# Kernel optimization log

Measured on AMD Instinct MI355X. Metric: run time of the kernel, lower is better.

Reference implementation:

```python
import jax, jax.numpy as jnp
import numpy as np

NDIM = 3
N = 192
DX = 1.0 / N          # uniform unit box
T_REF = 300.0         # reference temperature [K]
MU_REF = 1.8e-5       # reference viscosity [Pa s]
PR = 0.72             # Prandtl number
CP = 1005.0           # specific heat [J/kg/K]


def _ddx(f, axis):
    # 2nd-order central difference, periodic BC
    return (jnp.roll(f, -1, axis) - jnp.roll(f, 1, axis)) / (2.0 * DX)


def _gradient(f):
    # scalar [N,N,N] -> [NDIM, N,N,N]
    return jnp.stack([_ddx(f, a) for a in range(NDIM)], axis=0)


def _divergence(v):
    # vector [NDIM, N,N,N] -> [N,N,N]
    out = _ddx(v[0], 0)
    for a in range(1, NDIM):
        out = out + _ddx(v[a], a)
    return out


def _viscosity(T_dim):
    return MU_REF * (T_dim / T_REF) ** 0.7


def _conductivity(T_dim):
    return _viscosity(T_dim) * CP / PR


def setup_inputs() -> dict:
    key = jax.random.key(0)
    k1, k2 = jax.random.split(key)
    u = jax.random.normal(k1, (NDIM, N, N, N), dtype=jnp.float32)
    # nondimensional temperature, kept positive for the power-law viscosity
    T = jax.random.uniform(k2, (N, N, N), dtype=jnp.float32, minval=0.5, maxval=1.5)
    return {"u": u, "T": T}


def reference(u, T):
    # --- stress tensor ---
    mu = _viscosity(T * T_REF)                                   # [N,N,N]
    # gradu[i, j] = d u_i / d x_j
    gradu = jnp.stack([_gradient(u[i]) for i in range(NDIM)], 0)  # [3,3,N,N,N]
    divu = jnp.einsum('ii...->...', gradu)                        # trace -> [N,N,N]
    S = 0.5 * (gradu + jnp.swapaxes(gradu, 0, 1))                 # symmetrized
    eye = jnp.eye(NDIM, dtype=u.dtype)[:, :, None, None, None]
    tau = 2.0 * mu * S - (2.0 / 3.0) * mu * divu * eye            # [3,3,N,N,N]

    # --- heat flux ---
    k = _conductivity(T * T_REF)
    heat_flux = -k * _gradient(T)                                 # [3,N,N,N]

    # --- assemble RHS: [mass(=0), momentum(3), energy] ---
    momentum = jnp.stack([_divergence(tau[i]) for i in range(NDIM)], 0)
    energy = -_divergence(heat_flux)
    for i in range(NDIM):
        energy = energy + _divergence(tau[i] * u[i])
    zero = jnp.zeros_like(T)
    return jnp.concatenate([zero[None], momentum, energy[None]], axis=0)
```

## Files before the change

kernel.cpp:

```cpp
#include <hip/hip_runtime.h>

#define N  192
#define N2 (N * N)
#define N3 (N * N * N)

#define TX 32
#define TY 8
#define NT 256
#define ZC 12
#define GX (N / TX)
#define GY (N / TY)
#define GZ (N / ZC)
#define NBLK (GX * GY * GZ)
#define UX (TX + 4)
#define UY (TY + 4)
#define UP (UX * UY)
#define FX (TX + 2)
#define FY (TY + 2)
#define FP (FX * FY)

static constexpr float INV2DX     = (float)N / 2.0f;
static constexpr float SCALE2     = INV2DX * INV2DX;
static constexpr float MU_REF_F   = 1.8e-5f;
static constexpr float CP_OVER_PR = 1005.0f / 0.72f;
static constexpr float TWO_THIRDS = 2.0f / 3.0f;

__device__ __forceinline__ int wrapN(int a) {
    if (a < 0)  a += N;
    if (a >= N) a -= N;
    return a;
}

struct Flux { float t00, t01, t02, t11, t12, t22, F0, F1, F2; };

__device__ __forceinline__ Flux flux_eval_reg(const float4 zm, const float4 cc,
                                              const float4 zp,
                                              const float4* __restrict__ uC, int c)
{
    const float4 xp = uC[c + 1],  xm = uC[c - 1];
    const float4 yp = uC[c + UX], ym = uC[c - UX];

    const float d00 = zp.x - zm.x;
    const float d01 = yp.x - ym.x;
    const float d02 = xp.x - xm.x;
    const float d10 = zp.y - zm.y;
    const float d11 = yp.y - ym.y;
    const float d12 = xp.y - xm.y;
    const float d20 = zp.z - zm.z;
    const float d21 = yp.z - ym.z;
    const float d22 = xp.z - xm.z;
    const float dT0 = zp.w - zm.w;
    const float dT1 = yp.w - ym.w;
    const float dT2 = xp.w - xm.w;

    const float mu   = MU_REF_F * __powf(cc.w, 0.7f);
    const float mu2  = mu + mu;
    const float divu = d00 + d11 + d22;
    const float lam  = -TWO_THIRDS * mu * divu;

    Flux f;
    f.t00 = mu2 * d00 + lam;
    f.t11 = mu2 * d11 + lam;
    f.t22 = mu2 * d22 + lam;
    f.t01 = mu * (d01 + d10);
    f.t02 = mu * (d02 + d20);
    f.t12 = mu * (d12 + d21);
    const float kc = mu * CP_OVER_PR;
    f.F0 = kc * dT0 + f.t00 * cc.x + f.t01 * cc.y + f.t02 * cc.z;
    f.F1 = kc * dT1 + f.t01 * cc.x + f.t11 * cc.y + f.t12 * cc.z;
    f.F2 = kc * dT2 + f.t02 * cc.x + f.t12 * cc.y + f.t22 * cc.z;
    return f;
}

__device__ __forceinline__ Flux flux_eval_lds(const float4* __restrict__ uM,
                                              const float4* __restrict__ uC,
                                              const float4* __restrict__ uP, int c)
{
    return flux_eval_reg(uM[c], uC[c], uP[c], uC, c);
}

__device__ __forceinline__ void sf_store(float4* __restrict__ sY, float4* __restrict__ sX,
                                         int fi, const Flux& f)
{
    sY[fi] = make_float4(f.t01, f.t11, f.t12, f.F1);
    sX[fi] = make_float4(f.t02, f.t12, f.t22, f.F2);
}

__global__ __launch_bounds__(NT)
void diffusion_zmarch_kernel(const float* __restrict__ u,
                             const float* __restrict__ Tp,
                             float* __restrict__ out)
{
    __shared__ float4 su4[3][UP];
    __shared__ float4 sfY[FP];
    __shared__ float4 sfX[FP];

    const int id  = (int)blockIdx.x;
    const int nid = (id & 7) * (NBLK / 8) + (id >> 3);
    const int bzB = nid / (GX * GY);
    const int rem = nid % (GX * GY);
    const int bx  = (rem % GX) * TX;
    const int by  = (rem / GX) * TY;
    const int z0  = bzB * ZC;

    const int tx  = threadIdx.x & (TX - 1);
    const int ty  = threadIdx.x >> 5;
    const int tid = (int)threadIdx.x;

    const float* __restrict__ u0 = u;
    const float* __restrict__ u1 = u + N3;
    const float* __restrict__ u2 = u + 2 * N3;

    const int cu = (ty + 2) * UX + (tx + 2);
    const int fi = (ty + 1) * FX + (tx + 1);

    int hfx = -1, hfy = -1;
    if (tid < TX)                 { hfy = 0;      hfx = 1 + tid; }
    else if (tid < 2 * TX)        { hfy = FY - 1; hfx = 1 + tid - TX; }
    else if (tid < 2 * TX + TY)   { hfx = 0;      hfy = 1 + tid - 2 * TX; }
    else if (tid < 2 * (TX + TY)) { hfx = FX - 1; hfy = 1 + tid - 2 * TX - TY; }
    const bool hasH = (hfx >= 0);
    const int hcu = (hfy + 1) * UX + (hfx + 1);
    const int hfi = hfy * FX + hfx;

    const int  q0   = tid;
    const int  q1   = tid + NT;
    const bool has2 = (q1 < UP);
    int ro0, ro1 = 0;
    {
        const int ux = q0 % UX, uy = q0 / UX;
        ro0 = wrapN(by + uy - 2) * N + wrapN(bx + ux - 2);
    }
    if (has2) {
        const int ux = q1 % UX, uy = q1 / UX;
        ro1 = wrapN(by + uy - 2) * N + wrapN(bx + ux - 2);
    }

#define STAGE_DIRECT(slot, zw)                                              \
    do {                                                                    \
        const int base_ = (zw) * N2;                                        \
        {  const int g_ = base_ + ro0;                                      \
           su4[slot][q0] = make_float4(u0[g_], u1[g_], u2[g_], Tp[g_]); }   \
        if (has2) {                                                         \
           const int g_ = base_ + ro1;                                      \
           su4[slot][q1] = make_float4(u0[g_], u1[g_], u2[g_], Tp[g_]); }   \
    } while (0)

    STAGE_DIRECT(0, wrapN(z0 - 2));
    STAGE_DIRECT(1, wrapN(z0 - 1));
    STAGE_DIRECT(2, z0);
    __syncthreads();

    float t00m, t01m, t02m, F0m;
    {
        const Flux fM = flux_eval_lds(su4[0], su4[1], su4[2], cu);
        t00m = fM.t00; t01m = fM.t01; t02m = fM.t02; F0m = fM.F0;
    }
    __syncthreads();
    STAGE_DIRECT(0, z0 + 1);
    __syncthreads();

    float t00c, t01c, t02c, F0c;
    {
        const Flux fC = flux_eval_lds(su4[1], su4[2], su4[0], cu);
        t00c = fC.t00; t01c = fC.t01; t02c = fC.t02; F0c = fC.F0;
        sf_store(sfY, sfX, fi, fC);
        if (hasH) {
            const Flux h = flux_eval_lds(su4[1], su4[2], su4[0], hcu);
            sf_store(sfY, sfX, hfi, h);
        }
    }
    __syncthreads();
    STAGE_DIRECT(1, z0 + 2);
    __syncthreads();

    float4 rzm = su4[2][cu];
    float4 rcc = su4[0][cu];
    float4 hzm, hcc;
    if (hasH) { hzm = su4[2][hcu]; hcc = su4[0][hcu]; }

    float4 *pC = su4[0], *pP = su4[1], *pW = su4[2];

    int idx = z0 * N2 + (by + ty) * N + bx + tx;
    int zw  = z0 + 3; if (zw >= N) zw -= N;

    for (int it = 0; it < ZC; ++it) {
        const bool pref = (it <= ZC - 2);
        float4 r0, r1;
        if (pref) {
            const int base_ = zw * N2;
            { const int g_ = base_ + ro0;
              r0 = make_float4(u0[g_], u1[g_], u2[g_], Tp[g_]); }
            if (has2) {
              const int g_ = base_ + ro1;
              r1 = make_float4(u0[g_], u1[g_], u2[g_], Tp[g_]); }
        }

        const float4 yp = sfY[fi + FX], ym = sfY[fi - FX];
        const float4 xp = sfX[fi + 1],  xm = sfX[fi - 1];
        const float4 own = pP[cu];
        float4 hown;
        if (hasH) hown = pP[hcu];

        asm volatile("s_waitcnt lgkmcnt(0)\n\ts_barrier" ::: "memory");

        const Flux fp_ = flux_eval_reg(rzm, rcc, own, pC, cu);
        Flux h;
        if (hasH) h = flux_eval_reg(hzm, hcc, hown, pC, hcu);

        const float m0 = (fp_.t00 - t00m) + (yp.x - ym.x) + (xp.x - xm.x);
        const float m1 = (fp_.t01 - t01m) + (yp.y - ym.y) + (xp.y - xm.y);
        const float m2 = (fp_.t02 - t02m) + (yp.z - ym.z) + (xp.z - xm.z);
        const float en = (fp_.F0  - F0m)  + (yp.w - ym.w) + (xp.w - xm.w);

        sf_store(sfY, sfX, fi, fp_);
        if (hasH) sf_store(sfY, sfX, hfi, h);
        if (pref) { pW[q0] = r0; if (has2) pW[q1] = r1; }

        __builtin_nontemporal_store(m0 * SCALE2, &out[1 * N3 + idx]);
        __builtin_nontemporal_store(m1 * SCALE2, &out[2 * N3 + idx]);
        __builtin_nontemporal_store(m2 * SCALE2, &out[3 * N3 + idx]);
        __builtin_nontemporal_store(en * SCALE2, &out[4 * N3 + idx]);

        asm volatile("s_waitcnt lgkmcnt(0)\n\ts_barrier" ::: "memory");

        t00m = t00c; t01m = t01c; t02m = t02c; F0m = F0c;
        t00c = fp_.t00; t01c = fp_.t01; t02c = fp_.t02; F0c = fp_.F0;
        rzm = rcc; rcc = own;
        if (hasH) { hzm = hcc; hcc = hown; }
        float4* t = pC; pC = pP; pP = pW; pW = t;
        idx += N2;
        if (++zw >= N) zw = 0;
    }
#undef STAGE_DIRECT
}

extern "C" void kernel_launch(void* const* d_in, const int* in_sizes, int n_in,
                              void* d_out, int out_size, void* d_ws, size_t ws_size,
                              hipStream_t stream)
{
    const float* u   = (const float*)d_in[0];
    const float* T   = (const float*)d_in[1];
    float*       out = (float*)d_out;

    hipMemsetAsync(out, 0, (size_t)N3 * sizeof(float), stream);

    hipLaunchKernelGGL(diffusion_zmarch_kernel, dim3(NBLK), dim3(NT), 0, stream,
                       u, T, out);
}
```

Before: 101.4 us.

## Process two z-planes per march iteration with double-buffered flux tiles

Restructures the z-march so each loop iteration computes fluxes for two planes and writes two output planes, using a second pair of shared flux buffers. All LDS reads for both planes are hoisted before a single barrier, and two input planes are prefetched per iteration, halving the number of barrier pairs per block. It also adds a launch-bounds occupancy hint of 3 blocks. The cost is much higher register pressure from the extra live float4 neighbours and a larger shared-memory footprint, which may limit occupancy or cause spills.

```diff
diff --git a/kernel.cpp b/kernel.cpp
--- a/kernel.cpp
+++ b/kernel.cpp
@@ -8,6 +8,7 @@
 #define TY 8
 #define NT 256
 #define ZC 12
+#define NIT (ZC / 2)
 #define GX (N / TX)
 #define GY (N / TY)
 #define GZ (N / ZC)
@@ -33,13 +34,11 @@
 
 struct Flux { float t00, t01, t02, t11, t12, t22, F0, F1, F2; };
 
-__device__ __forceinline__ Flux flux_eval_reg(const float4 zm, const float4 cc,
-                                              const float4 zp,
-                                              const float4* __restrict__ uC, int c)
-{
-    const float4 xp = uC[c + 1],  xm = uC[c - 1];
-    const float4 yp = uC[c + UX], ym = uC[c - UX];
-
+__device__ __forceinline__ Flux flux_eval(const float4 zm, const float4 cc,
+                                          const float4 zp,
+                                          const float4 xp, const float4 xm,
+                                          const float4 yp, const float4 ym)
+{
     const float d00 = zp.x - zm.x;
     const float d01 = yp.x - ym.x;
     const float d02 = xp.x - xm.x;
@@ -72,28 +71,22 @@
     return f;
 }
 
-__device__ __forceinline__ Flux flux_eval_lds(const float4* __restrict__ uM,
-                                              const float4* __restrict__ uC,
-                                              const float4* __restrict__ uP, int c)
-{
-    return flux_eval_reg(uM[c], uC[c], uP[c], uC, c);
-}
-
-__device__ __forceinline__ void sf_store(float4* __restrict__ sY, float4* __restrict__ sX,
-                                         int fi, const Flux& f)
-{
-    sY[fi] = make_float4(f.t01, f.t11, f.t12, f.F1);
-    sX[fi] = make_float4(f.t02, f.t12, f.t22, f.F2);
-}
-
-__global__ __launch_bounds__(NT)
-void diffusion_zmarch_kernel(const float* __restrict__ u,
-                             const float* __restrict__ Tp,
-                             float* __restrict__ out)
+__device__ __forceinline__ Flux flux_eval_at(const float4* __restrict__ uM,
+                                             const float4* __restrict__ uC,
+                                             const float4* __restrict__ uP, int c)
+{
+    return flux_eval(uM[c], uC[c], uP[c], uC[c + 1], uC[c - 1],
+                     uC[c + UX], uC[c - UX]);
+}
+
+__global__ __launch_bounds__(NT, 3)
+void diffusion_zmarch2_kernel(const float* __restrict__ u,
+                              const float* __restrict__ Tp,
+                              float* __restrict__ out)
 {
     __shared__ float4 su4[3][UP];
-    __shared__ float4 sfY[FP];
-    __shared__ float4 sfX[FP];
+    __shared__ float4 sfAY[FP], sfAX[FP];
+    __shared__ float4 sfBY[FP], sfBX[FP];
 
     const int id  = (int)blockIdx.x;
     const int nid = (id & 7) * (NBLK / 8) + (id >> 3);
@@ -153,7 +146,7 @@
 
     float t00m, t01m, t02m, F0m;
     {
-        const Flux fM = flux_eval_lds(su4[0], su4[1], su4[2], cu);
+        const Flux fM = flux_eval_at(su4[0], su4[1], su4[2], cu);
         t00m = fM.t00; t01m = fM.t01; t02m = fM.t02; F0m = fM.F0;
     }
     __syncthreads();
@@ -161,76 +154,120 @@
     __syncthreads();
 
     float t00c, t01c, t02c, F0c;
+    float4 rA, rB;
+    float4 hA = make_float4(0,0,0,0), hB = make_float4(0,0,0,0);
     {
-        const Flux fC = flux_eval_lds(su4[1], su4[2], su4[0], cu);
+        const Flux fC = flux_eval_at(su4[1], su4[2], su4[0], cu);
         t00c = fC.t00; t01c = fC.t01; t02c = fC.t02; F0c = fC.F0;
-        sf_store(sfY, sfX, fi, fC);
-        if (hasH) {
-            const Flux h = flux_eval_lds(su4[1], su4[2], su4[0], hcu);
-            sf_store(sfY, sfX, hfi, h);
-        }
+        sfAY[fi] = make_float4(fC.t01, fC.t11, fC.t12, fC.F1);
+        sfAX[fi] = make_float4(fC.t02, fC.t12, fC.t22, fC.F2);
+        if (hasH) {
+            const Flux h = flux_eval_at(su4[1], su4[2], su4[0], hcu);
+            sfAY[hfi] = make_float4(h.t01, h.t11, h.t12, h.F1);
+            sfAX[hfi] = make_float4(h.t02, h.t12, h.t22, h.F2);
+            hA = su4[2][hcu];
+            hB = su4[0][hcu];
+        }
+        rA = su4[2][cu];
+        rB = su4[0][cu];
     }
     __syncthreads();
     STAGE_DIRECT(1, z0 + 2);
-    __syncthreads();
-
-    float4 rzm = su4[2][cu];
-    float4 rcc = su4[0][cu];
-    float4 hzm, hcc;
-    if (hasH) { hzm = su4[2][hcu]; hcc = su4[0][hcu]; }
-
-    float4 *pC = su4[0], *pP = su4[1], *pW = su4[2];
+    STAGE_DIRECT(2, z0 + 3);
+    __syncthreads();
+
+    float4 *pA = su4[0], *pB = su4[1], *pC = su4[2];
 
     int idx = z0 * N2 + (by + ty) * N + bx + tx;
-    int zw  = z0 + 3; if (zw >= N) zw -= N;
-
-    for (int it = 0; it < ZC; ++it) {
-        const bool pref = (it <= ZC - 2);
-        float4 r0, r1;
+
+    for (int k = 0; k < NIT; ++k) {
+        const int  z    = z0 + 2 * k;
+        const bool pref = (k < NIT - 1);
+
+        float4 r4a, r4b, r5a, r5b;
         if (pref) {
-            const int base_ = zw * N2;
-            { const int g_ = base_ + ro0;
-              r0 = make_float4(u0[g_], u1[g_], u2[g_], Tp[g_]); }
-            if (has2) {
-              const int g_ = base_ + ro1;
-              r1 = make_float4(u0[g_], u1[g_], u2[g_], Tp[g_]); }
-        }
-
-        const float4 yp = sfY[fi + FX], ym = sfY[fi - FX];
-        const float4 xp = sfX[fi + 1],  xm = sfX[fi - 1];
-        const float4 own = pP[cu];
-        float4 hown;
-        if (hasH) hown = pP[hcu];
+            const int za = wrapN(z + 4), zb = wrapN(z + 5);
+            { const int g = za * N2 + ro0;
+              r4a = make_float4(u0[g], u1[g], u2[g], Tp[g]); }
+            if (has2) { const int g = za * N2 + ro1;
+              r4b = make_float4(u0[g], u1[g], u2[g], Tp[g]); }
+            { const int g = zb * N2 + ro0;
+              r5a = make_float4(u0[g], u1[g], u2[g], Tp[g]); }
+            if (has2) { const int g = zb * N2 + ro1;
+              r5b = make_float4(u0[g], u1[g], u2[g], Tp[g]); }
+        }
+
+        const float4 ayp = sfAY[fi + FX], aym = sfAY[fi - FX];
+        const float4 axp = sfAX[fi + 1],  axm = sfAX[fi - 1];
+        const float4 oB  = pB[cu];
+        const float4 oC  = pC[cu];
+        const float4 xpa = pA[cu + 1],  xma = pA[cu - 1];
+        const float4 ypa = pA[cu + UX], yma = pA[cu - UX];
+        const float4 xpb = pB[cu + 1],  xmb = pB[cu - 1];
+        const float4 ypb = pB[cu + UX], ymb = pB[cu - UX];
+        float4 hoB, hoC, hxpa, hxma, hypa, hyma, hxpb, hxmb, hypb, hymb;
+        if (hasH) {
+            hoB  = pB[hcu];       hoC  = pC[hcu];
+            hxpa = pA[hcu + 1];   hxma = pA[hcu - 1];
+            hypa = pA[hcu + UX];  hyma = pA[hcu - UX];
+            hxpb = pB[hcu + 1];   hxmb = pB[hcu - 1];
+            hypb = pB[hcu + UX];  hymb = pB[hcu - UX];
+        }
 
         asm volatile("s_waitcnt lgkmcnt(0)\n\ts_barrier" ::: "memory");
 
-        const Flux fp_ = flux_eval_reg(rzm, rcc, own, pC, cu);
-        Flux h;
-        if (hasH) h = flux_eval_reg(hzm, hcc, hown, pC, hcu);
-
-        const float m0 = (fp_.t00 - t00m) + (yp.x - ym.x) + (xp.x - xm.x);
-        const float m1 = (fp_.t01 - t01m) + (yp.y - ym.y) + (xp.y - xm.y);
-        const float m2 = (fp_.t02 - t02m) + (yp.z - ym.z) + (xp.z - xm.z);
-        const float en = (fp_.F0  - F0m)  + (yp.w - ym.w) + (xp.w - xm.w);
-
-        sf_store(sfY, sfX, fi, fp_);
-        if (hasH) sf_store(sfY, sfX, hfi, h);
-        if (pref) { pW[q0] = r0; if (has2) pW[q1] = r1; }
-
-        __builtin_nontemporal_store(m0 * SCALE2, &out[1 * N3 + idx]);
-        __builtin_nontemporal_store(m1 * SCALE2, &out[2 * N3 + idx]);
-        __builtin_nontemporal_store(m2 * SCALE2, &out[3 * N3 + idx]);
-        __builtin_nontemporal_store(en * SCALE2, &out[4 * N3 + idx]);
+        const Flux P1 = flux_eval(rA, rB, oB, xpa, xma, ypa, yma);
+        const Flux P2 = flux_eval(rB, oB, oC, xpb, xmb, ypb, ymb);
+        Flux H1, H2;
+        if (hasH) {
+            H1 = flux_eval(hA, hB, hoB, hxpa, hxma, hypa, hyma);
+            H2 = flux_eval(hB, hoB, hoC, hxpb, hxmb, hypb, hymb);
+        }
+
+        sfBY[fi] = make_float4(P1.t01, P1.t11, P1.t12, P1.F1);
+        sfBX[fi] = make_float4(P1.t02, P1.t12, P1.t22, P1.F2);
+        sfAY[fi] = make_float4(P2.t01, P2.t11, P2.t12, P2.F1);
+        sfAX[fi] = make_float4(P2.t02, P2.t12, P2.t22, P2.F2);
+        if (hasH) {
+            sfBY[hfi] = make_float4(H1.t01, H1.t11, H1.t12, H1.F1);
+            sfBX[hfi] = make_float4(H1.t02, H1.t12, H1.t22, H1.F2);
+            sfAY[hfi] = make_float4(H2.t01, H2.t11, H2.t12, H2.F1);
+            sfAX[hfi] = make_float4(H2.t02, H2.t12, H2.t22, H2.F2);
+        }
+        if (pref) {
+            pA[q0] = r4a; if (has2) pA[q1] = r4b;
+            pB[q0] = r5a; if (has2) pB[q1] = r5b;
+        }
+
+        const float m0a = (P1.t00 - t00m) + (ayp.x - aym.x) + (axp.x - axm.x);
+        const float m1a = (P1.t01 - t01m) + (ayp.y - aym.y) + (axp.y - axm.y);
+        const float m2a = (P1.t02 - t02m) + (ayp.z - aym.z) + (axp.z - axm.z);
+        const float ena = (P1.F0  - F0m)  + (ayp.w - aym.w) + (axp.w - axm.w);
+        __builtin_nontemporal_store(m0a * SCALE2, &out[1 * N3 + idx]);
+        __builtin_nontemporal_store(m1a * SCALE2, &out[2 * N3 + idx]);
+        __builtin_nontemporal_store(m2a * SCALE2, &out[3 * N3 + idx]);
+        __builtin_nontemporal_store(ena * SCALE2, &out[4 * N3 + idx]);
 
         asm volatile("s_waitcnt lgkmcnt(0)\n\ts_barrier" ::: "memory");
 
-        t00m = t00c; t01m = t01c; t02m = t02c; F0m = F0c;
-        t00c = fp_.t00; t01c = fp_.t01; t02c = fp_.t02; F0c = fp_.F0;
-        rzm = rcc; rcc = own;
-        if (hasH) { hzm = hcc; hcc = hown; }
-        float4* t = pC; pC = pP; pP = pW; pW = t;
-        idx += N2;
-        if (++zw >= N) zw = 0;
+        const float4 byp = sfBY[fi + FX], bym = sfBY[fi - FX];
+        const float4 bxp = sfBX[fi + 1],  bxm = sfBX[fi - 1];
+        const float m0b = (P2.t00 - t00c) + (byp.x - bym.x) + (bxp.x - bxm.x);
+        const float m1b = (P2.t01 - t01c) + (byp.y - bym.y) + (bxp.y - bxm.y);
+        const float m2b = (P2.t02 - t02c) + (byp.z - bym.z) + (bxp.z - bxm.z);
+        const float enb = (P2.F0  - F0c)  + (byp.w - bym.w) + (bxp.w - bxm.w);
+        const int idx1 = idx + N2;
+        __builtin_nontemporal_store(m0b * SCALE2, &out[1 * N3 + idx1]);
+        __builtin_nontemporal_store(m1b * SCALE2, &out[2 * N3 + idx1]);
+        __builtin_nontemporal_store(m2b * SCALE2, &out[3 * N3 + idx1]);
+        __builtin_nontemporal_store(enb * SCALE2, &out[4 * N3 + idx1]);
+
+        t00m = P1.t00; t01m = P1.t01; t02m = P1.t02; F0m = P1.F0;
+        t00c = P2.t00; t01c = P2.t01; t02c = P2.t02; F0c = P2.F0;
+        rA = oB; rB = oC;
+        if (hasH) { hA = hoB; hB = hoC; }
+        float4* t = pA; pA = pC; pC = pB; pB = t;
+        idx += 2 * N2;
     }
 #undef STAGE_DIRECT
 }
@@ -245,6 +282,6 @@
 
     hipMemsetAsync(out, 0, (size_t)N3 * sizeof(float), stream);
 
-    hipLaunchKernelGGL(diffusion_zmarch_kernel, dim3(NBLK), dim3(NT), 0, stream,
+    hipLaunchKernelGGL(diffusion_zmarch2_kernel, dim3(NBLK), dim3(NT), 0, stream,
                        u, T, out);
 }
```

After: 192.9 us. +90.2%, slower.
